# Kernel tuning notes

Hardware: AMD Instinct MI355X
Metric: run time of the kernel (lower is better)

The kernel has to match this reference:

```python
import jax, jax.numpy as jnp
import numpy as np

B, T, N, C = 1, 2, 10000, 64
H, Co = 4, 64
E = 160000
NEG_SLOPE = 0.2
LN_EPS = 1e-5


def setup_inputs() -> dict:
    key = jax.random.key(0)
    ks = jax.random.split(key, 8)
    s_in = 1.0 / np.sqrt(C)
    s_att = 1.0 / np.sqrt(Co)
    s_proj = 1.0 / np.sqrt(H * Co)
    return {
        "x": jax.random.normal(ks[0], (B, T, N, C), jnp.float32),
        "edge_index": jax.random.randint(ks[1], (2, E), 0, N, dtype=jnp.int32),
        "W_l": jax.random.normal(ks[2], (C, H * Co), jnp.float32) * s_in,
        "b_l": jnp.zeros((H * Co,), jnp.float32),
        "W_r": jax.random.normal(ks[3], (C, H * Co), jnp.float32) * s_in,
        "b_r": jnp.zeros((H * Co,), jnp.float32),
        "att": jax.random.normal(ks[4], (H, Co), jnp.float32) * s_att,
        "bias": jnp.zeros((H * Co,), jnp.float32),
        "W_proj": jax.random.normal(ks[5], (H * Co, Co), jnp.float32) * s_proj,
        "b_proj": jnp.zeros((Co,), jnp.float32),
        "ln_gamma": jnp.ones((Co,), jnp.float32),
        "ln_beta": jnp.zeros((Co,), jnp.float32),
    }


def reference(x, edge_index, W_l, b_l, W_r, b_r, att, bias, W_proj, b_proj, ln_gamma, ln_beta):
    src, dst = edge_index[0], edge_index[1]
    # node transforms: [B,T,N,H,Co]
    x_l = (x @ W_l + b_l).reshape(B, T, N, H, Co)
    x_r = (x @ W_r + b_r).reshape(B, T, N, H, Co)
    # per-edge gathers: [B,T,E,H,Co]
    x_j = x_l[:, :, src]  # source-side features (messages)
    x_i = x_r[:, :, dst]  # target-side features
    m = jax.nn.leaky_relu(x_i + x_j, NEG_SLOPE)
    alpha = jnp.einsum('bteho,ho->bteh', m, att)  # [B,T,E,H]
    # segment softmax over edges grouped by target node (edge axis leading)
    a = jnp.moveaxis(alpha, 2, 0)  # [E,B,T,H]
    amax = jax.lax.stop_gradient(jax.ops.segment_max(a, dst, num_segments=N))
    a = jnp.exp(a - amax[dst])
    denom = jax.ops.segment_sum(a, dst, num_segments=N)
    attn = a / denom[dst]  # [E,B,T,H]
    # weighted messages scattered to target nodes
    msg = jnp.moveaxis(x_j, 2, 0) * attn[..., None]  # [E,B,T,H,Co]
    agg = jax.ops.segment_sum(msg, dst, num_segments=N)  # [N,B,T,H,Co]
    out = jnp.moveaxis(agg, 0, 2).reshape(B, T, N, H * Co) + bias
    x_mha = jax.nn.relu(out)
    # projection + identity residual (in_channels == out_channels)
    x_sam = x_mha @ W_proj + b_proj + x
    mu = jnp.mean(x_sam, axis=-1, keepdims=True)
    var = jnp.var(x_sam, axis=-1, keepdims=True)
    y = (x_sam - mu) * jax.lax.rsqrt(var + LN_EPS) * ln_gamma + ln_beta
    return jax.nn.relu(y)
```

## Files before the change

### kernel.cpp

```cpp
#include <hip/hip_runtime.h>

#define T_  2
#define N_  10000
#define C_  64
#define H_  4
#define Co_ 64
#define E_  160000
#define HC_ 256
#define PAD_ 48
#define NEG_SLOPE 0.2f
#define LN_EPS 1e-5f
#define SCAT_BLOCKS (E_ / 256)
#define GEMM_BLOCKS (T_ * N_ / 32)

typedef float v2f __attribute__((ext_vector_type(2)));

#if __has_builtin(__builtin_elementwise_fma)
#define PKFMA(a, b, c) __builtin_elementwise_fma((a), (b), (c))
#else
#define PKFMA(a, b, c) ((a) * (b) + (c))
#endif

__device__ __forceinline__ v2f v2(float x, float y) { v2f r; r.x = x; r.y = y; return r; }
__device__ __forceinline__ v2f sp(float x) { v2f r; r.x = x; r.y = x; return r; }

__device__ __forceinline__ float bf2f(unsigned short u) {
    return __uint_as_float((unsigned)u << 16);
}
__device__ __forceinline__ unsigned short f2bf(float f) {
    const unsigned u = __float_as_uint(f);
    return (unsigned short)((u + 0x7FFFu + ((u >> 16) & 1u)) >> 16);
}
__device__ __forceinline__ float4 u2f4(ushort4 u) {
    return make_float4(bf2f(u.x), bf2f(u.y), bf2f(u.z), bf2f(u.w));
}

__device__ __forceinline__ void red16x4(float& p0, float& p1, float& p2, float& p3) {
    asm("s_nop 1\n\t"
        "v_add_f32_dpp %0, %0, %0 quad_perm:[1,0,3,2] row_mask:0xf bank_mask:0xf\n\t"
        "v_add_f32_dpp %1, %1, %1 quad_perm:[1,0,3,2] row_mask:0xf bank_mask:0xf\n\t"
        "v_add_f32_dpp %2, %2, %2 quad_perm:[1,0,3,2] row_mask:0xf bank_mask:0xf\n\t"
        "v_add_f32_dpp %3, %3, %3 quad_perm:[1,0,3,2] row_mask:0xf bank_mask:0xf\n\t"
        "v_add_f32_dpp %0, %0, %0 quad_perm:[2,3,0,1] row_mask:0xf bank_mask:0xf\n\t"
        "v_add_f32_dpp %1, %1, %1 quad_perm:[2,3,0,1] row_mask:0xf bank_mask:0xf\n\t"
        "v_add_f32_dpp %2, %2, %2 quad_perm:[2,3,0,1] row_mask:0xf bank_mask:0xf\n\t"
        "v_add_f32_dpp %3, %3, %3 quad_perm:[2,3,0,1] row_mask:0xf bank_mask:0xf\n\t"
        "v_add_f32_dpp %0, %0, %0 row_half_mirror row_mask:0xf bank_mask:0xf\n\t"
        "v_add_f32_dpp %1, %1, %1 row_half_mirror row_mask:0xf bank_mask:0xf\n\t"
        "v_add_f32_dpp %2, %2, %2 row_half_mirror row_mask:0xf bank_mask:0xf\n\t"
        "v_add_f32_dpp %3, %3, %3 row_half_mirror row_mask:0xf bank_mask:0xf\n\t"
        "v_add_f32_dpp %0, %0, %0 row_mirror row_mask:0xf bank_mask:0xf\n\t"
        "v_add_f32_dpp %1, %1, %1 row_mirror row_mask:0xf bank_mask:0xf\n\t"
        "v_add_f32_dpp %2, %2, %2 row_mirror row_mask:0xf bank_mask:0xf\n\t"
        "v_add_f32_dpp %3, %3, %3 row_mirror row_mask:0xf bank_mask:0xf"
        : "+v"(p0), "+v"(p1), "+v"(p2), "+v"(p3));
}

__device__ __forceinline__ float edot2(const v2f xa, const v2f xb,
                                       const v2f aa, const v2f ab, const float4 c) {
    v2f u = v2(c.x, c.y) + xa;
    v2f v = v2(c.z, c.w) + xb;
    v2f lu = __builtin_elementwise_max(u, u * 0.2f);
    v2f lv = __builtin_elementwise_max(v, v * 0.2f);
    v2f p = PKFMA(lv, ab, lu * aa);
    return p.x + p.y;
}

__device__ __forceinline__ void group_update(
        const v2f xa, const v2f xb, const v2f aa, const v2f ab,
        const float4 c0, const float4 c1, const float4 c2, const float4 c3,
        int k, int cnt, float& m, float& s, float4& acc) {
    float p0 = edot2(xa, xb, aa, ab, c0);
    float p1 = edot2(xa, xb, aa, ab, c1);
    float p2 = edot2(xa, xb, aa, ab, c2);
    float p3 = edot2(xa, xb, aa, ab, c3);
    red16x4(p0, p1, p2, p3);
    if (k + 1 >= cnt) p1 = -INFINITY;
    if (k + 2 >= cnt) p2 = -INFINITY;
    if (k + 3 >= cnt) p3 = -INFINITY;
    const float gm = fmaxf(fmaxf(p0, p1), fmaxf(p2, p3));
    const float mn = fmaxf(m, gm);
    const float sc = __expf(m - mn);
    const float w0 = __expf(p0 - mn);
    const float w1 = __expf(p1 - mn);
    const float w2 = __expf(p2 - mn);
    const float w3 = __expf(p3 - mn);
    s = fmaf(s, sc, w0 + w1 + w2 + w3);
    v2f q01 = v2(c3.x, c3.y) * w3;
    q01 = PKFMA(v2(c2.x, c2.y), sp(w2), q01);
    q01 = PKFMA(v2(c1.x, c1.y), sp(w1), q01);
    q01 = PKFMA(v2(c0.x, c0.y), sp(w0), q01);
    v2f r01 = PKFMA(v2(acc.x, acc.y), sp(sc), q01);
    v2f q23 = v2(c3.z, c3.w) * w3;
    q23 = PKFMA(v2(c2.z, c2.w), sp(w2), q23);
    q23 = PKFMA(v2(c1.z, c1.w), sp(w1), q23);
    q23 = PKFMA(v2(c0.z, c0.w), sp(w0), q23);
    v2f r23 = PKFMA(v2(acc.z, acc.w), sp(sc), q23);
    acc.x = r01.x; acc.y = r01.y; acc.z = r23.x; acc.w = r23.y;
    m = mn;
}

__global__ __launch_bounds__(256) void scat_gemm(
        const int* __restrict__ src, const int* __restrict__ dst,
        int* __restrict__ cursor, unsigned short* __restrict__ perm,
        const float* __restrict__ x, const float* __restrict__ Wl,
        const float* __restrict__ bl, const float* __restrict__ Wr,
        const float* __restrict__ br, unsigned short* __restrict__ xlb,
        float* __restrict__ xr) {
    __shared__ float4 xs[32 * 16];
    const int tid = threadIdx.x;
    if (blockIdx.x < SCAT_BLOCKS) {
        const int e = blockIdx.x * 256 + tid;
        const int d = dst[e];
        const int pos = atomicAdd(&cursor[d], 1);
        if (pos < PAD_) perm[d * PAD_ + pos] = (unsigned short)src[e];
        return;
    }
    const int r0 = (blockIdx.x - SCAT_BLOCKS) * 32;
    xs[tid]       = ((const float4*)(x + (size_t)r0 * C_))[tid];
    xs[256 + tid] = ((const float4*)(x + (size_t)r0 * C_))[256 + tid];
    __syncthreads();

    const int wv    = tid >> 6;
    const int mat   = wv >> 1;
    const int rbase = (wv & 1) << 4;
    const int col4  = tid & 63;
    const float* W  = mat ? Wr : Wl;
    const float4 b4 = ((const float4*)(mat ? br : bl))[col4];

    v2f accA[16], accB[16];
    #pragma unroll
    for (int r = 0; r < 16; ++r) { accA[r] = v2(b4.x, b4.y); accB[r] = v2(b4.z, b4.w); }

    #pragma unroll 2
    for (int c4 = 0; c4 < 16; ++c4) {
        const float4 w0 = ((const float4*)(W + (size_t)(c4 * 4 + 0) * HC_))[col4];
        const float4 w1 = ((const float4*)(W + (size_t)(c4 * 4 + 1) * HC_))[col4];
        const float4 w2 = ((const float4*)(W + (size_t)(c4 * 4 + 2) * HC_))[col4];
        const float4 w3 = ((const float4*)(W + (size_t)(c4 * 4 + 3) * HC_))[col4];
        const v2f w0A = v2(w0.x, w0.y), w0B = v2(w0.z, w0.w);
        const v2f w1A = v2(w1.x, w1.y), w1B = v2(w1.z, w1.w);
        const v2f w2A = v2(w2.x, w2.y), w2B = v2(w2.z, w2.w);
        const v2f w3A = v2(w3.x, w3.y), w3B = v2(w3.z, w3.w);
        #pragma unroll
        for (int r = 0; r < 16; ++r) {
            const float4 xv = xs[(rbase + r) * 16 + c4];
            accA[r] = PKFMA(sp(xv.x), w0A, accA[r]);
            accB[r] = PKFMA(sp(xv.x), w0B, accB[r]);
            accA[r] = PKFMA(sp(xv.y), w1A, accA[r]);
            accB[r] = PKFMA(sp(xv.y), w1B, accB[r]);
            accA[r] = PKFMA(sp(xv.z), w2A, accA[r]);
            accB[r] = PKFMA(sp(xv.z), w2B, accB[r]);
            accA[r] = PKFMA(sp(xv.w), w3A, accA[r]);
            accB[r] = PKFMA(sp(xv.w), w3B, accB[r]);
        }
    }
    if (mat) {
        #pragma unroll
        for (int r = 0; r < 16; ++r) {
            float4 o4;
            o4.x = accA[r].x; o4.y = accA[r].y; o4.z = accB[r].x; o4.w = accB[r].y;
            ((float4*)(xr + (size_t)(r0 + rbase + r) * HC_))[col4] = o4;
        }
    } else {
        #pragma unroll
        for (int r = 0; r < 16; ++r) {
            ushort4 u;
            u.x = f2bf(accA[r].x); u.y = f2bf(accA[r].y);
            u.z = f2bf(accB[r].x); u.w = f2bf(accB[r].y);
            ((ushort4*)(xlb + (size_t)(r0 + rbase + r) * HC_))[col4] = u;
        }
    }
}

__global__ __launch_bounds__(256, 4) void node_proj(
        const unsigned short* __restrict__ xlb, const float* __restrict__ xr,
        const float* __restrict__ att, const unsigned short* __restrict__ perm,
        const int* __restrict__ cursor, const float* __restrict__ bias,
        const float* __restrict__ Wp, const float* __restrict__ bp,
        const float* __restrict__ x, const float* __restrict__ gamma,
        const float* __restrict__ beta, float* __restrict__ out) {
    __shared__ float sh_act[8][HC_];
    __shared__ float sh_part[4][8][Co_];
    const int wv   = threadIdx.x >> 6;
    const int lane = threadIdx.x & 63;
    const int n    = blockIdx.x * 4 + wv;
    const int deg  = min(cursor[n], PAD_);
    const float4 av  = ((const float4*)att)[lane];
    const float4 xi0 = ((const float4*)&xr[(size_t)n * HC_])[lane];
    const float4 xi1 = ((const float4*)&xr[((size_t)N_ + n) * HC_])[lane];
    const int myidx  = (lane < deg) ? (int)perm[n * PAD_ + lane] : 0;
    const unsigned short* xl1 = xlb + (size_t)N_ * HC_;

    const v2f xa = v2(xi0.x, xi0.y), xb = v2(xi0.z, xi0.w);
    const v2f ya = v2(xi1.x, xi1.y), yb = v2(xi1.z, xi1.w);
    const v2f aa = v2(av.x, av.y),   ab = v2(av.z, av.w);

    float m0 = -INFINITY, s0 = 0.f, m1 = -INFINITY, s1 = 0.f;
    float4 a0 = make_float4(0.f, 0.f, 0.f, 0.f), a1 = a0;

    ushort4 b0, b1, b2, b3, b4, b5, b6, b7;
    auto fetch = [&](int kk) {
        const int i0 = __builtin_amdgcn_readlane(myidx, kk + 0);
        const int i1 = __builtin_amdgcn_readlane(myidx, kk + 1);
        const int i2 = __builtin_amdgcn_readlane(myidx, kk + 2);
        const int i3 = __builtin_amdgcn_readlane(myidx, kk + 3);
        b0 = ((const ushort4*)&xlb[(size_t)i0 * HC_])[lane];
        b1 = ((const ushort4*)&xlb[(size_t)i1 * HC_])[lane];
        b2 = ((const ushort4*)&xlb[(size_t)i2 * HC_])[lane];
        b3 = ((const ushort4*)&xlb[(size_t)i3 * HC_])[lane];
        b4 = ((const ushort4*)&xl1[(size_t)i0 * HC_])[lane];
        b5 = ((const ushort4*)&xl1[(size_t)i1 * HC_])[lane];
        b6 = ((const ushort4*)&xl1[(size_t)i2 * HC_])[lane];
        b7 = ((const ushort4*)&xl1[(size_t)i3 * HC_])[lane];
    };
    if (deg > 0) fetch(0);
    for (int k = 0; k < deg; k += 4) {
        const float4 c0 = u2f4(b0), c1 = u2f4(b1), c2 = u2f4(b2), c3 = u2f4(b3);
        const float4 d0 = u2f4(b4), d1 = u2f4(b5), d2 = u2f4(b6), d3 = u2f4(b7);
        if (k + 4 < deg) fetch(k + 4);
        group_update(xa, xb, aa, ab, c0, c1, c2, c3, k, deg, m0, s0, a0);
        group_update(ya, yb, aa, ab, d0, d1, d2, d3, k, deg, m1, s1, a1);
    }

    const float4 bias4 = ((const float4*)bias)[lane];
    {
        const float i0v = (deg > 0) ? 1.f / s0 : 0.f;
        const float i1v = (deg > 0) ? 1.f / s1 : 0.f;
        float4 v;
        v.x = fmaxf(fmaf(a0.x, i0v, bias4.x), 0.f);
        v.y = fmaxf(fmaf(a0.y, i0v, bias4.y), 0.f);
        v.z = fmaxf(fmaf(a0.z, i0v, bias4.z), 0.f);
        v.w = fmaxf(fmaf(a0.w, i0v, bias4.w), 0.f);
        ((float4*)&sh_act[2 * wv + 0][0])[lane] = v;
        v.x = fmaxf(fmaf(a1.x, i1v, bias4.x), 0.f);
        v.y = fmaxf(fmaf(a1.y, i1v, bias4.y), 0.f);
        v.z = fmaxf(fmaf(a1.z, i1v, bias4.z), 0.f);
        v.w = fmaxf(fmaf(a1.w, i1v, bias4.w), 0.f);
        ((float4*)&sh_act[2 * wv + 1][0])[lane] = v;
    }
    __syncthreads();

    v2f part[8];
    #pragma unroll
    for (int r = 0; r < 8; ++r) part[r] = v2(0.f, 0.f);
    {
        const int kq = wv * 16;
        #pragma unroll 4
        for (int k4 = 0; k4 < 16; ++k4) {
            const int k = (kq + k4) * 4;
            const float w0 = Wp[(size_t)(k + 0) * Co_ + lane];
            const float w1 = Wp[(size_t)(k + 1) * Co_ + lane];
            const float w2 = Wp[(size_t)(k + 2) * Co_ + lane];
            const float w3 = Wp[(size_t)(k + 3) * Co_ + lane];
            const v2f w01 = v2(w0, w1), w23 = v2(w2, w3);
            #pragma unroll
            for (int r = 0; r < 8; ++r) {
                const float4 a = ((const float4*)&sh_act[r][0])[kq + k4];
                part[r] = PKFMA(v2(a.x, a.y), w01, part[r]);
                part[r] = PKFMA(v2(a.z, a.w), w23, part[r]);
            }
        }
    }
    #pragma unroll
    for (int r = 0; r < 8; ++r) sh_part[wv][r][lane] = part[r].x + part[r].y;
    __syncthreads();

    const int o = lane;
    const float bpo = bp[o];
    float p0 = sh_part[0][2 * wv + 0][o] + sh_part[1][2 * wv + 0][o]
             + sh_part[2][2 * wv + 0][o] + sh_part[3][2 * wv + 0][o]
             + bpo + x[(size_t)n * C_ + o];
    float p1 = sh_part[0][2 * wv + 1][o] + sh_part[1][2 * wv + 1][o]
             + sh_part[2][2 * wv + 1][o] + sh_part[3][2 * wv + 1][o]
             + bpo + x[((size_t)N_ + n) * C_ + o];

    const float go = gamma[o], bo = beta[o];
    {
        float s1r = p0;
        #pragma unroll
        for (int off = 1; off < 64; off <<= 1) s1r += __shfl_xor(s1r, off, 64);
        const float mu0 = s1r * (1.f / 64.f);
        const float dv0 = p0 - mu0;
        float s2r = dv0 * dv0;
        #pragma unroll
        for (int off = 1; off < 64; off <<= 1) s2r += __shfl_xor(s2r, off, 64);
        out[(size_t)n * C_ + o] =
            fmaxf(dv0 * rsqrtf(s2r * (1.f / 64.f) + LN_EPS) * go + bo, 0.f);

        float t1r = p1;
        #pragma unroll
        for (int off = 1; off < 64; off <<= 1) t1r += __shfl_xor(t1r, off, 64);
        const float mu1 = t1r * (1.f / 64.f);
        const float dv1 = p1 - mu1;
        float t2r = dv1 * dv1;
        #pragma unroll
        for (int off = 1; off < 64; off <<= 1) t2r += __shfl_xor(t2r, off, 64);
        out[((size_t)N_ + n) * C_ + o] =
            fmaxf(dv1 * rsqrtf(t2r * (1.f / 64.f) + LN_EPS) * go + bo, 0.f);
    }
}

extern "C" void kernel_launch(void* const* d_in, const int* in_sizes, int n_in,
                              void* d_out, int out_size, void* d_ws, size_t ws_size,
                              hipStream_t stream) {
    const float* x    = (const float*)d_in[0];
    const int*   ei   = (const int*)  d_in[1];
    const float* Wl   = (const float*)d_in[2];
    const float* bl   = (const float*)d_in[3];
    const float* Wr   = (const float*)d_in[4];
    const float* br   = (const float*)d_in[5];
    const float* att  = (const float*)d_in[6];
    const float* bias = (const float*)d_in[7];
    const float* Wp   = (const float*)d_in[8];
    const float* bp   = (const float*)d_in[9];
    const float* gam  = (const float*)d_in[10];
    const float* bet  = (const float*)d_in[11];
    const int* src = ei;
    const int* dst = ei + E_;

    char* ws = (char*)d_ws;
    unsigned short* xlb  = (unsigned short*)ws;
    float*          xr   = (float*)(xlb + (size_t)T_ * N_ * HC_);
    int*            cursor = (int*)(xr + (size_t)T_ * N_ * HC_);
    unsigned short* perm   = (unsigned short*)(cursor + N_);

    hipMemsetAsync(cursor, 0, N_ * sizeof(int), stream);
    scat_gemm<<<SCAT_BLOCKS + GEMM_BLOCKS, 256, 0, stream>>>(
        src, dst, cursor, perm, x, Wl, bl, Wr, br, xlb, xr);
    node_proj<<<N_ / 4, 256, 0, stream>>>(xlb, xr, att, perm, cursor, bias,
                                          Wp, bp, x, gam, bet, (float*)d_out);
}
```

Before: 164.4 us.

## Split node_proj work per timestep into one 128-thread block per node

Each node now gets its own 128-thread block, and each of its two wavefronts handles one timestep. Before, a 256-thread block handled four nodes and each wavefront covered both timesteps. The gather loop keeps two independent 4-edge fetch buffers in flight so more loads overlap with compute. The intent is to cut per-wave serial latency and raise memory-level parallelism. The cost is that each block loads Wp for only one node, so weight traffic per node goes up, and there are more, smaller blocks.

New measurement: 161.0 us. 2.1% less time.

```diff
diff --git a/kernel.cpp b/kernel.cpp
--- a/kernel.cpp
+++ b/kernel.cpp
@@ -173,132 +173,115 @@
     }
 }
 
-__global__ __launch_bounds__(256, 4) void node_proj(
+__global__ __launch_bounds__(128, 6) void node_proj(
         const unsigned short* __restrict__ xlb, const float* __restrict__ xr,
         const float* __restrict__ att, const unsigned short* __restrict__ perm,
         const int* __restrict__ cursor, const float* __restrict__ bias,
         const float* __restrict__ Wp, const float* __restrict__ bp,
         const float* __restrict__ x, const float* __restrict__ gamma,
         const float* __restrict__ beta, float* __restrict__ out) {
-    __shared__ float sh_act[8][HC_];
-    __shared__ float sh_part[4][8][Co_];
-    const int wv   = threadIdx.x >> 6;
+    __shared__ float sh_act[T_][HC_];
+    __shared__ float sh_part[T_][T_][Co_];
+    const int t    = threadIdx.x >> 6;
     const int lane = threadIdx.x & 63;
-    const int n    = blockIdx.x * 4 + wv;
+    const int n    = blockIdx.x;
     const int deg  = min(cursor[n], PAD_);
-    const float4 av  = ((const float4*)att)[lane];
-    const float4 xi0 = ((const float4*)&xr[(size_t)n * HC_])[lane];
-    const float4 xi1 = ((const float4*)&xr[((size_t)N_ + n) * HC_])[lane];
-    const int myidx  = (lane < deg) ? (int)perm[n * PAD_ + lane] : 0;
-    const unsigned short* xl1 = xlb + (size_t)N_ * HC_;
-
-    const v2f xa = v2(xi0.x, xi0.y), xb = v2(xi0.z, xi0.w);
-    const v2f ya = v2(xi1.x, xi1.y), yb = v2(xi1.z, xi1.w);
-    const v2f aa = v2(av.x, av.y),   ab = v2(av.z, av.w);
-
-    float m0 = -INFINITY, s0 = 0.f, m1 = -INFINITY, s1 = 0.f;
-    float4 a0 = make_float4(0.f, 0.f, 0.f, 0.f), a1 = a0;
-
-    ushort4 b0, b1, b2, b3, b4, b5, b6, b7;
-    auto fetch = [&](int kk) {
+    const float4 av = ((const float4*)att)[lane];
+    const float4 xi = ((const float4*)&xr[((size_t)t * N_ + n) * HC_])[lane];
+    const int myidx = (lane < deg) ? (int)perm[n * PAD_ + lane] : 0;
+    const unsigned short* xlt = xlb + (size_t)t * N_ * HC_;
+
+    const v2f xa = v2(xi.x, xi.y), xb = v2(xi.z, xi.w);
+    const v2f aa = v2(av.x, av.y), ab = v2(av.z, av.w);
+
+    float m = -INFINITY, s = 0.f;
+    float4 acc = make_float4(0.f, 0.f, 0.f, 0.f);
+
+    ushort4 A0, A1, A2, A3, B0, B1, B2, B3;
+    auto fetchA = [&](int kk) {
         const int i0 = __builtin_amdgcn_readlane(myidx, kk + 0);
         const int i1 = __builtin_amdgcn_readlane(myidx, kk + 1);
         const int i2 = __builtin_amdgcn_readlane(myidx, kk + 2);
         const int i3 = __builtin_amdgcn_readlane(myidx, kk + 3);
-        b0 = ((const ushort4*)&xlb[(size_t)i0 * HC_])[lane];
-        b1 = ((const ushort4*)&xlb[(size_t)i1 * HC_])[lane];
-        b2 = ((const ushort4*)&xlb[(size_t)i2 * HC_])[lane];
-        b3 = ((const ushort4*)&xlb[(size_t)i3 * HC_])[lane];
-        b4 = ((const ushort4*)&xl1[(size_t)i0 * HC_])[lane];
-        b5 = ((const ushort4*)&xl1[(size_t)i1 * HC_])[lane];
-        b6 = ((const ushort4*)&xl1[(size_t)i2 * HC_])[lane];
-        b7 = ((const ushort4*)&xl1[(size_t)i3 * HC_])[lane];
+        A0 = ((const ushort4*)&xlt[(size_t)i0 * HC_])[lane];
+        A1 = ((const ushort4*)&xlt[(size_t)i1 * HC_])[lane];
+        A2 = ((const ushort4*)&xlt[(size_t)i2 * HC_])[lane];
+        A3 = ((const ushort4*)&xlt[(size_t)i3 * HC_])[lane];
     };
-    if (deg > 0) fetch(0);
-    for (int k = 0; k < deg; k += 4) {
-        const float4 c0 = u2f4(b0), c1 = u2f4(b1), c2 = u2f4(b2), c3 = u2f4(b3);
-        const float4 d0 = u2f4(b4), d1 = u2f4(b5), d2 = u2f4(b6), d3 = u2f4(b7);
-        if (k + 4 < deg) fetch(k + 4);
-        group_update(xa, xb, aa, ab, c0, c1, c2, c3, k, deg, m0, s0, a0);
-        group_update(ya, yb, aa, ab, d0, d1, d2, d3, k, deg, m1, s1, a1);
-    }
-
-    const float4 bias4 = ((const float4*)bias)[lane];
+    auto fetchB = [&](int kk) {
+        const int i0 = __builtin_amdgcn_readlane(myidx, kk + 0);
+        const int i1 = __builtin_amdgcn_readlane(myidx, kk + 1);
+        const int i2 = __builtin_amdgcn_readlane(myidx, kk + 2);
+        const int i3 = __builtin_amdgcn_readlane(myidx, kk + 3);
+        B0 = ((const ushort4*)&xlt[(size_t)i0 * HC_])[lane];
+        B1 = ((const ushort4*)&xlt[(size_t)i1 * HC_])[lane];
+        B2 = ((const ushort4*)&xlt[(size_t)i2 * HC_])[lane];
+        B3 = ((const ushort4*)&xlt[(size_t)i3 * HC_])[lane];
+    };
+    if (deg > 0) fetchA(0);
+    if (deg > 4) fetchB(4);
+    for (int k = 0; k < deg; k += 8) {
+        {
+            const float4 c0 = u2f4(A0), c1 = u2f4(A1), c2 = u2f4(A2), c3 = u2f4(A3);
+            if (k + 8 < deg) fetchA(k + 8);
+            group_update(xa, xb, aa, ab, c0, c1, c2, c3, k, deg, m, s, acc);
+        }
+        if (k + 4 < deg) {
+            const float4 c0 = u2f4(B0), c1 = u2f4(B1), c2 = u2f4(B2), c3 = u2f4(B3);
+            if (k + 12 < deg) fetchB(k + 12);
+            group_update(xa, xb, aa, ab, c0, c1, c2, c3, k + 4, deg, m, s, acc);
+        }
+    }
+
     {
-        const float i0v = (deg > 0) ? 1.f / s0 : 0.f;
-        const float i1v = (deg > 0) ? 1.f / s1 : 0.f;
+        const float4 bias4 = ((const float4*)bias)[lane];
+        const float inv = (deg > 0) ? 1.f / s : 0.f;
         float4 v;
-        v.x = fmaxf(fmaf(a0.x, i0v, bias4.x), 0.f);
-        v.y = fmaxf(fmaf(a0.y, i0v, bias4.y), 0.f);
-        v.z = fmaxf(fmaf(a0.z, i0v, bias4.z), 0.f);
-        v.w = fmaxf(fmaf(a0.w, i0v, bias4.w), 0.f);
-        ((float4*)&sh_act[2 * wv + 0][0])[lane] = v;
-        v.x = fmaxf(fmaf(a1.x, i1v, bias4.x), 0.f);
-        v.y = fmaxf(fmaf(a1.y, i1v, bias4.y), 0.f);
-        v.z = fmaxf(fmaf(a1.z, i1v, bias4.z), 0.f);
-        v.w = fmaxf(fmaf(a1.w, i1v, bias4.w), 0.f);
-        ((float4*)&sh_act[2 * wv + 1][0])[lane] = v;
+        v.x = fmaxf(fmaf(acc.x, inv, bias4.x), 0.f);
+        v.y = fmaxf(fmaf(acc.y, inv, bias4.y), 0.f);
+        v.z = fmaxf(fmaf(acc.z, inv, bias4.z), 0.f);
+        v.w = fmaxf(fmaf(acc.w, inv, bias4.w), 0.f);
+        ((float4*)&sh_act[t][0])[lane] = v;
     }
     __syncthreads();
 
-    v2f part[8];
-    #pragma unroll
-    for (int r = 0; r < 8; ++r) part[r] = v2(0.f, 0.f);
+    v2f P0 = v2(0.f, 0.f), P1 = v2(0.f, 0.f);
     {
-        const int kq = wv * 16;
+        const int kq = t * 32;
         #pragma unroll 4
-        for (int k4 = 0; k4 < 16; ++k4) {
+        for (int k4 = 0; k4 < 32; ++k4) {
             const int k = (kq + k4) * 4;
             const float w0 = Wp[(size_t)(k + 0) * Co_ + lane];
             const float w1 = Wp[(size_t)(k + 1) * Co_ + lane];
             const float w2 = Wp[(size_t)(k + 2) * Co_ + lane];
             const float w3 = Wp[(size_t)(k + 3) * Co_ + lane];
             const v2f w01 = v2(w0, w1), w23 = v2(w2, w3);
-            #pragma unroll
-            for (int r = 0; r < 8; ++r) {
-                const float4 a = ((const float4*)&sh_act[r][0])[kq + k4];
-                part[r] = PKFMA(v2(a.x, a.y), w01, part[r]);
-                part[r] = PKFMA(v2(a.z, a.w), w23, part[r]);
-            }
-        }
-    }
+            const float4 a0 = ((const float4*)&sh_act[0][0])[kq + k4];
+            const float4 a1 = ((const float4*)&sh_act[1][0])[kq + k4];
+            P0 = PKFMA(v2(a0.x, a0.y), w01, P0);
+            P0 = PKFMA(v2(a0.z, a0.w), w23, P0);
+            P1 = PKFMA(v2(a1.x, a1.y), w01, P1);
+            P1 = PKFMA(v2(a1.z, a1.w), w23, P1);
+        }
+    }
+    sh_part[t][0][lane] = P0.x + P0.y;
+    sh_part[t][1][lane] = P1.x + P1.y;
+    __syncthreads();
+
+    const int o = lane;
+    float p = sh_part[0][t][o] + sh_part[1][t][o]
+            + bp[o] + x[((size_t)t * N_ + n) * C_ + o];
+    const float go = gamma[o], bo = beta[o];
+    float s1r = p;
     #pragma unroll
-    for (int r = 0; r < 8; ++r) sh_part[wv][r][lane] = part[r].x + part[r].y;
-    __syncthreads();
-
-    const int o = lane;
-    const float bpo = bp[o];
-    float p0 = sh_part[0][2 * wv + 0][o] + sh_part[1][2 * wv + 0][o]
-             + sh_part[2][2 * wv + 0][o] + sh_part[3][2 * wv + 0][o]
-             + bpo + x[(size_t)n * C_ + o];
-    float p1 = sh_part[0][2 * wv + 1][o] + sh_part[1][2 * wv + 1][o]
-             + sh_part[2][2 * wv + 1][o] + sh_part[3][2 * wv + 1][o]
-             + bpo + x[((size_t)N_ + n) * C_ + o];
-
-    const float go = gamma[o], bo = beta[o];
-    {
-        float s1r = p0;
-        #pragma unroll
-        for (int off = 1; off < 64; off <<= 1) s1r += __shfl_xor(s1r, off, 64);
-        const float mu0 = s1r * (1.f / 64.f);
-        const float dv0 = p0 - mu0;
-        float s2r = dv0 * dv0;
-        #pragma unroll
-        for (int off = 1; off < 64; off <<= 1) s2r += __shfl_xor(s2r, off, 64);
-        out[(size_t)n * C_ + o] =
-            fmaxf(dv0 * rsqrtf(s2r * (1.f / 64.f) + LN_EPS) * go + bo, 0.f);
-
-        float t1r = p1;
-        #pragma unroll
-        for (int off = 1; off < 64; off <<= 1) t1r += __shfl_xor(t1r, off, 64);
-        const float mu1 = t1r * (1.f / 64.f);
-        const float dv1 = p1 - mu1;
-        float t2r = dv1 * dv1;
-        #pragma unroll
-        for (int off = 1; off < 64; off <<= 1) t2r += __shfl_xor(t2r, off, 64);
-        out[((size_t)N_ + n) * C_ + o] =
-            fmaxf(dv1 * rsqrtf(t2r * (1.f / 64.f) + LN_EPS) * go + bo, 0.f);
-    }
+    for (int off = 1; off < 64; off <<= 1) s1r += __shfl_xor(s1r, off, 64);
+    const float mu = s1r * (1.f / 64.f);
+    const float dv = p - mu;
+    float s2r = dv * dv;
+    #pragma unroll
+    for (int off = 1; off < 64; off <<= 1) s2r += __shfl_xor(s2r, off, 64);
+    out[((size_t)t * N_ + n) * C_ + o] =
+        fmaxf(dv * rsqrtf(s2r * (1.f / 64.f) + LN_EPS) * go + bo, 0.f);
 }
 
 extern "C" void kernel_launch(void* const* d_in, const int* in_sizes, int n_in,
@@ -328,6 +311,6 @@
     hipMemsetAsync(cursor, 0, N_ * sizeof(int), stream);
     scat_gemm<<<SCAT_BLOCKS + GEMM_BLOCKS, 256, 0, stream>>>(
         src, dst, cursor, perm, x, Wl, bl, Wr, br, xlb, xr);
-    node_proj<<<N_ / 4, 256, 0, stream>>>(xlb, xr, att, perm, cursor, bias,
-                                          Wp, bp, x, gam, bet, (float*)d_out);
-}
+    node_proj<<<N_, 128, 0, stream>>>(xlb, xr, att, perm, cursor, bias,
+                                      Wp, bp, x, gam, bet, (float*)d_out);
+}
```
